# Optimization experiments

Hardware: AMD Instinct MI355X
Metric: run time of the kernel (lower is better)

## Reference

```python
import jax, jax.numpy as jnp
import numpy as np

N_NODES = 50000
N_EDGES = 1600000
D_IN = 512
D_OUT = 512


def setup_inputs() -> dict:
    key = jax.random.key(0)
    k1, k2, k3, k4, k5 = jax.random.split(key, 5)
    inputs = jax.random.normal(k1, (N_NODES, D_IN), dtype=jnp.float32)
    # xavier_uniform for weight [D_IN, D_OUT]
    limit = float(np.sqrt(6.0 / (D_IN + D_OUT)))
    weight = jax.random.uniform(k2, (D_IN, D_OUT), dtype=jnp.float32, minval=-limit, maxval=limit)
    adj_rows = jnp.sort(jax.random.randint(k3, (N_EDGES,), 0, N_NODES, dtype=jnp.int32))
    adj_cols = jax.random.randint(k4, (N_EDGES,), 0, N_NODES, dtype=jnp.int32)
    adj_vals = jax.random.uniform(k5, (N_EDGES,), dtype=jnp.float32)
    return {"inputs": inputs, "weight": weight, "adj_rows": adj_rows,
            "adj_cols": adj_cols, "adj_vals": adj_vals}


def reference(inputs, weight, adj_rows, adj_cols, adj_vals):
    # dropout(p=0.0) is identity in this configuration
    support = inputs @ weight                      # [N, D_OUT] dense GEMM
    gathered = support[adj_cols] * adj_vals[:, None]   # [E, D_OUT]
    output = jax.ops.segment_sum(gathered, adj_rows, num_segments=N_NODES)  # spmm
    return output
```

## Files before the change

### kernel.cpp

```cpp
#include <hip/hip_runtime.h>
#include <hip/hip_bf16.h>

#define N_NODES 50000
#define N_EDGES 1600000
#define D 512

typedef __attribute__((ext_vector_type(8))) short short8;
typedef __attribute__((ext_vector_type(4))) float f32x4;
typedef __attribute__((ext_vector_type(2))) float f32x2;
typedef __attribute__((ext_vector_type(8))) unsigned short u16x8;

__device__ __forceinline__ void async_copy16(const void* g, void* l) {
    __builtin_amdgcn_global_load_lds(
        (const __attribute__((address_space(1))) unsigned int*)g,
        (__attribute__((address_space(3))) unsigned int*)l, 16, 0, 0);
}

__global__ __launch_bounds__(256) void cvt_kernel(const float* __restrict__ X,
                                                  unsigned short* __restrict__ Xb) {
    size_t idx = (size_t)(blockIdx.x * 256 + threadIdx.x) * 8;
    f32x4 v0 = *(const f32x4*)(X + idx);
    f32x4 v1 = *(const f32x4*)(X + idx + 4);
    u16x8 u;
#pragma unroll
    for (int k = 0; k < 4; ++k) {
        u[k]     = __bfloat16_as_ushort(__float2bfloat16(v0[k]));
        u[k + 4] = __bfloat16_as_ushort(__float2bfloat16(v1[k]));
    }
    *(u16x8*)(Xb + idx) = u;
}

__global__ __launch_bounds__(256) void wt_kernel(const float* __restrict__ W,
                                                 unsigned short* __restrict__ Wt) {
    int idx = blockIdx.x * 256 + threadIdx.x;
    int k = idx >> 9;
    int n = idx & 511;
    Wt[n * D + k] = __bfloat16_as_ushort(__float2bfloat16(W[k * D + n]));
}

__global__ __launch_bounds__(256) void rowptr_kernel(const int* __restrict__ rows,
                                                     int* __restrict__ row_start) {
    int r = blockIdx.x * 256 + threadIdx.x;
    if (r > N_NODES) return;
    int lo = 0, hi = N_EDGES;
    while (lo < hi) {
        int mid = (lo + hi) >> 1;
        if (rows[mid] < r) lo = mid + 1; else hi = mid;
    }
    row_start[r] = lo;
}

__global__ __launch_bounds__(256) void gemm_kernel(const unsigned short* __restrict__ Xb,
                                                   const unsigned short* __restrict__ Wt,
                                                   __hip_bfloat16* __restrict__ support) {
    __shared__ unsigned short As[128 * 32];
    __shared__ unsigned short Bs[128 * 32];

    const int t = threadIdx.x;
    const int lane = t & 63;
    const int wave = t >> 6;
    const int wm = (wave & 1) * 64;
    const int wn = (wave >> 1) * 64;
    const int m0 = blockIdx.x * 128;
    const int n0 = blockIdx.y * 128;
    const int l15 = lane & 15;
    const int quad = lane >> 4;

    f32x4 acc[4][4];
#pragma unroll
    for (int i = 0; i < 4; ++i)
#pragma unroll
        for (int j = 0; j < 4; ++j) acc[i][j] = (f32x4)(0.0f);

    const int srow = t >> 2;
    const int skb = (t & 3) * 8;
    int gra = m0 + srow;        if (gra > N_NODES - 1) gra = N_NODES - 1;
    int grb = m0 + 64 + srow;   if (grb > N_NODES - 1) grb = N_NODES - 1;
    const size_t aoff0 = (size_t)gra * D + skb;
    const size_t aoff1 = (size_t)grb * D + skb;
    const size_t boff0 = (size_t)(n0 + srow) * D + skb;
    const size_t boff1 = (size_t)(n0 + 64 + srow) * D + skb;
    unsigned short* lA = As + t * 8;
    unsigned short* lB = Bs + t * 8;

    for (int kt = 0; kt < D / 32; ++kt) {
        const int k0 = kt * 32;
        async_copy16(Xb + aoff0 + k0, lA);
        async_copy16(Xb + aoff1 + k0, lA + 2048);
        async_copy16(Wt + boff0 + k0, lB);
        async_copy16(Wt + boff1 + k0, lB + 2048);
        __syncthreads();

        short8 af[4], bf[4];
#pragma unroll
        for (int i = 0; i < 4; ++i) af[i] = *(const short8*)(As + (wm + i * 16 + l15) * 32 + quad * 8);
#pragma unroll
        for (int j = 0; j < 4; ++j) bf[j] = *(const short8*)(Bs + (wn + j * 16 + l15) * 32 + quad * 8);
#pragma unroll
        for (int i = 0; i < 4; ++i)
#pragma unroll
            for (int j = 0; j < 4; ++j)
                acc[i][j] = __builtin_amdgcn_mfma_f32_16x16x32_bf16(af[i], bf[j], acc[i][j], 0, 0, 0);
        __syncthreads();
    }

#pragma unroll
    for (int i = 0; i < 4; ++i) {
        int grow = m0 + wm + i * 16 + quad * 4;
#pragma unroll
        for (int j = 0; j < 4; ++j) {
            int gc = n0 + wn + j * 16 + l15;
#pragma unroll
            for (int rr = 0; rr < 4; ++rr) {
                int gr = grow + rr;
                if (gr < N_NODES)
                    support[(size_t)gr * D + gc] = __float2bfloat16(acc[i][j][rr]);
            }
        }
    }
}

__global__ __launch_bounds__(256) void spmm_kernel(const unsigned short* __restrict__ support,
                                                   const int* __restrict__ cols,
                                                   const float* __restrict__ vals,
                                                   const int* __restrict__ row_start,
                                                   float* __restrict__ out) {
    const int r = blockIdx.x;
    const int t = threadIdx.x;
    const int s = row_start[r];
    const int e = row_start[r + 1];
    const size_t co = 2 * t;

    float ax = 0.f, ay = 0.f;
    int i = s;
    for (; i + 8 <= e; i += 8) {
        int c[8]; float v[8]; unsigned int h[8];
#pragma unroll
        for (int k = 0; k < 8; ++k) { c[k] = cols[i + k]; v[k] = vals[i + k]; }
#pragma unroll
        for (int k = 0; k < 8; ++k)
            h[k] = *(const unsigned int*)(support + (size_t)c[k] * D + co);
#pragma unroll
        for (int k = 0; k < 8; ++k) {
            ax += v[k] * __uint_as_float(h[k] << 16);
            ay += v[k] * __uint_as_float(h[k] & 0xffff0000u);
        }
    }
    for (; i < e; ++i) {
        int c = cols[i];
        float v = vals[i];
        unsigned int h = *(const unsigned int*)(support + (size_t)c * D + co);
        ax += v * __uint_as_float(h << 16);
        ay += v * __uint_as_float(h & 0xffff0000u);
    }
    f32x2 o; o[0] = ax; o[1] = ay;
    __builtin_nontemporal_store(o, (f32x2*)(out + (size_t)r * D + co));
}

extern "C" void kernel_launch(void* const* d_in, const int* in_sizes, int n_in,
                              void* d_out, int out_size, void* d_ws, size_t ws_size,
                              hipStream_t stream) {
    (void)in_sizes; (void)n_in; (void)out_size; (void)ws_size;
    const float* X    = (const float*)d_in[0];
    const float* W    = (const float*)d_in[1];
    const int* rows   = (const int*)d_in[2];
    const int* cols   = (const int*)d_in[3];
    const float* vals = (const float*)d_in[4];
    float* out = (float*)d_out;

    unsigned short* support = (unsigned short*)d_ws;
    unsigned short* Wt      = support + (size_t)N_NODES * D;
    int* row_start          = (int*)(Wt + (size_t)D * D);
    unsigned short* Xb = (unsigned short*)d_out;

    cvt_kernel<<<12500, 256, 0, stream>>>(X, Xb);
    wt_kernel<<<(D * D) / 256, 256, 0, stream>>>(W, Wt);
    rowptr_kernel<<<(N_NODES + 256) / 256, 256, 0, stream>>>(rows, row_start);

    dim3 gg((N_NODES + 127) / 128, D / 128);
    gemm_kernel<<<gg, 256, 0, stream>>>(Xb, Wt, (__hip_bfloat16*)support);

    spmm_kernel<<<N_NODES, 256, 0, stream>>>(support, cols, vals, row_start, out);
}
```

Baseline: 460.5 us.

## Map one wavefront per row in SpMM with 16-byte gathers

The SpMM kernel now assigns each 64-lane wavefront one output row, with each lane handling 8 columns via 16-byte loads, instead of one 256-thread block per row with 4-byte loads. This cuts the number of edge index/value loads per row by a factor of four and widens the gather transactions. Edges are unrolled by 4 instead of 8, so fewer gathers are in flight per thread. Work may also be less balanced across waves in the same block.

Measured after the change: 473.1 us. 2.7% more time.

```diff
diff --git a/kernel.cpp b/kernel.cpp
--- a/kernel.cpp
+++ b/kernel.cpp
@@ -120,41 +120,54 @@
     }
 }
 
+__device__ __forceinline__ void fma8(float* acc, uint4 h, float v) {
+#pragma unroll
+    for (int d = 0; d < 4; ++d) {
+        unsigned int w = (&h.x)[d];
+        acc[2 * d]     += v * __uint_as_float(w << 16);
+        acc[2 * d + 1] += v * __uint_as_float(w & 0xffff0000u);
+    }
+}
+
 __global__ __launch_bounds__(256) void spmm_kernel(const unsigned short* __restrict__ support,
                                                    const int* __restrict__ cols,
                                                    const float* __restrict__ vals,
                                                    const int* __restrict__ row_start,
                                                    float* __restrict__ out) {
-    const int r = blockIdx.x;
     const int t = threadIdx.x;
+    const int lane = t & 63;
+    const int wave = t >> 6;
+    const int r = blockIdx.x * 4 + wave;
     const int s = row_start[r];
     const int e = row_start[r + 1];
-    const size_t co = 2 * t;
+    const int co = lane * 8;
 
-    float ax = 0.f, ay = 0.f;
+    float acc[8];
+#pragma unroll
+    for (int k = 0; k < 8; ++k) acc[k] = 0.f;
+
     int i = s;
-    for (; i + 8 <= e; i += 8) {
-        int c[8]; float v[8]; unsigned int h[8];
+    for (; i + 4 <= e; i += 4) {
+        int c[4]; float v[4]; uint4 h[4];
 #pragma unroll
-        for (int k = 0; k < 8; ++k) { c[k] = cols[i + k]; v[k] = vals[i + k]; }
+        for (int k = 0; k < 4; ++k) { c[k] = cols[i + k]; v[k] = vals[i + k]; }
 #pragma unroll
-        for (int k = 0; k < 8; ++k)
-            h[k] = *(const unsigned int*)(support + (size_t)c[k] * D + co);
+        for (int k = 0; k < 4; ++k)
+            h[k] = *(const uint4*)(support + (size_t)c[k] * D + co);
 #pragma unroll
-        for (int k = 0; k < 8; ++k) {
-            ax += v[k] * __uint_as_float(h[k] << 16);
-            ay += v[k] * __uint_as_float(h[k] & 0xffff0000u);
-        }
+        for (int k = 0; k < 4; ++k) fma8(acc, h[k], v[k]);
     }
     for (; i < e; ++i) {
-        int c = cols[i];
-        float v = vals[i];
-        unsigned int h = *(const unsigned int*)(support + (size_t)c * D + co);
-        ax += v * __uint_as_float(h << 16);
-        ay += v * __uint_as_float(h & 0xffff0000u);
+        uint4 h = *(const uint4*)(support + (size_t)cols[i] * D + co);
+        fma8(acc, h, vals[i]);
     }
-    f32x2 o; o[0] = ax; o[1] = ay;
-    __builtin_nontemporal_store(o, (f32x2*)(out + (size_t)r * D + co));
+
+    f32x4 o0, o1;
+#pragma unroll
+    for (int k = 0; k < 4; ++k) { o0[k] = acc[k]; o1[k] = acc[k + 4]; }
+    float* op = out + (size_t)r * D + co;
+    __builtin_nontemporal_store(o0, (f32x4*)op);
+    __builtin_nontemporal_store(o1, (f32x4*)(op + 4));
 }
 
 extern "C" void kernel_launch(void* const* d_in, const int* in_sizes, int n_in,
@@ -180,5 +193,5 @@
     dim3 gg((N_NODES + 127) / 128, D / 128);
     gemm_kernel<<<gg, 256, 0, stream>>>(Xb, Wt, (__hip_bfloat16*)support);
 
-    spmm_kernel<<<N_NODES, 256, 0, stream>>>(support, cols, vals, row_start, out);
+    spmm_kernel<<<12500, 256, 0, stream>>>(support, cols, vals, row_start, out);
 }
```

## Fuse fp32-to-bf16 conversion into double-buffered GEMM with 128x256 tiles

Applied to the files above, without the earlier changes.

Drops the separate input conversion kernel. The GEMM now loads fp32 X directly, converts it to bf16 in registers and writes it to LDS. The GEMM also double-buffers its LDS tiles so that next-tile loads overlap the MFMA work, and moves to 512-thread blocks computing 128x256 tiles, which halves the reloads of the X tile. The aim is to remove the round trip of the bf16 X copy through memory and to hide load latency, at the cost of more LDS and register pressure per block.

Result: faster. 446.1 us (-3.1%).

```diff
diff --git a/kernel.cpp b/kernel.cpp
--- a/kernel.cpp
+++ b/kernel.cpp
@@ -14,20 +14,6 @@
     __builtin_amdgcn_global_load_lds(
         (const __attribute__((address_space(1))) unsigned int*)g,
         (__attribute__((address_space(3))) unsigned int*)l, 16, 0, 0);
-}
-
-__global__ __launch_bounds__(256) void cvt_kernel(const float* __restrict__ X,
-                                                  unsigned short* __restrict__ Xb) {
-    size_t idx = (size_t)(blockIdx.x * 256 + threadIdx.x) * 8;
-    f32x4 v0 = *(const f32x4*)(X + idx);
-    f32x4 v1 = *(const f32x4*)(X + idx + 4);
-    u16x8 u;
-#pragma unroll
-    for (int k = 0; k < 4; ++k) {
-        u[k]     = __bfloat16_as_ushort(__float2bfloat16(v0[k]));
-        u[k + 4] = __bfloat16_as_ushort(__float2bfloat16(v1[k]));
-    }
-    *(u16x8*)(Xb + idx) = u;
 }
 
 __global__ __launch_bounds__(256) void wt_kernel(const float* __restrict__ W,
@@ -50,19 +36,24 @@
     row_start[r] = lo;
 }
 
-__global__ __launch_bounds__(256) void gemm_kernel(const unsigned short* __restrict__ Xb,
-                                                   const unsigned short* __restrict__ Wt,
-                                                   __hip_bfloat16* __restrict__ support) {
-    __shared__ unsigned short As[128 * 32];
-    __shared__ unsigned short Bs[128 * 32];
+#define BM 128
+#define BN 256
+#define BK 32
+
+__global__ __launch_bounds__(512, 4) void gemm_kernel(const float* __restrict__ X,
+                                                      const unsigned short* __restrict__ Wt,
+                                                      __hip_bfloat16* __restrict__ support) {
+    __shared__ unsigned short As[2][BM * BK];
+    __shared__ unsigned short Bs[2][BN * BK];
 
     const int t = threadIdx.x;
     const int lane = t & 63;
-    const int wave = t >> 6;
-    const int wm = (wave & 1) * 64;
-    const int wn = (wave >> 1) * 64;
-    const int m0 = blockIdx.x * 128;
-    const int n0 = blockIdx.y * 128;
+    const int w = t >> 6;
+    const int wm = (w >> 2) * 64;
+    const int wn = (w & 3) * 64;
+    const int bid = blockIdx.x;
+    const int m0 = (bid >> 1) * BM;
+    const int n0 = (bid & 1) * BN;
     const int l15 = lane & 15;
     const int quad = lane >> 4;
 
@@ -72,36 +63,69 @@
 #pragma unroll
         for (int j = 0; j < 4; ++j) acc[i][j] = (f32x4)(0.0f);
 
-    const int srow = t >> 2;
-    const int skb = (t & 3) * 8;
-    int gra = m0 + srow;        if (gra > N_NODES - 1) gra = N_NODES - 1;
-    int grb = m0 + 64 + srow;   if (grb > N_NODES - 1) grb = N_NODES - 1;
-    const size_t aoff0 = (size_t)gra * D + skb;
-    const size_t aoff1 = (size_t)grb * D + skb;
-    const size_t boff0 = (size_t)(n0 + srow) * D + skb;
-    const size_t boff1 = (size_t)(n0 + 64 + srow) * D + skb;
-    unsigned short* lA = As + t * 8;
-    unsigned short* lB = Bs + t * 8;
-
-    for (int kt = 0; kt < D / 32; ++kt) {
-        const int k0 = kt * 32;
-        async_copy16(Xb + aoff0 + k0, lA);
-        async_copy16(Xb + aoff1 + k0, lA + 2048);
-        async_copy16(Wt + boff0 + k0, lB);
-        async_copy16(Wt + boff1 + k0, lB + 2048);
-        __syncthreads();
+    int arow = m0 + (t >> 2);
+    if (arow > N_NODES - 1) arow = N_NODES - 1;
+    const float* abase = X + (size_t)arow * D + (t & 3) * 8;
+    const int awr = (t >> 2) * BK + (t & 3) * 8;
+
+
+    {
+        f32x4 a0 = *(const f32x4*)abase;
+        f32x4 a1 = *(const f32x4*)(abase + 4);
+#pragma unroll
+        for (int c = 0; c < 2; ++c) {
+            int cid = c * 512 + t;
+            async_copy16(Wt + (size_t)(n0 + (cid >> 2)) * D + (cid & 3) * 8,
+                         &Bs[0][cid * 8]);
+        }
+        u16x8 u;
+#pragma unroll
+        for (int k = 0; k < 4; ++k) {
+            u[k]     = __bfloat16_as_ushort(__float2bfloat16(a0[k]));
+            u[k + 4] = __bfloat16_as_ushort(__float2bfloat16(a1[k]));
+        }
+        *(u16x8*)(&As[0][awr]) = u;
+    }
+    __syncthreads();
+
+    int cur = 0;
+    for (int kt = 0; kt < D / BK; ++kt) {
+        f32x4 a0n, a1n;
+        const int nxt = cur ^ 1;
+        if (kt < D / BK - 1) {
+            const int k0n = (kt + 1) * BK;
+            a0n = *(const f32x4*)(abase + k0n);
+            a1n = *(const f32x4*)(abase + k0n + 4);
+#pragma unroll
+            for (int c = 0; c < 2; ++c) {
+                int cid = c * 512 + t;
+                async_copy16(Wt + (size_t)(n0 + (cid >> 2)) * D + k0n + (cid & 3) * 8,
+                             &Bs[nxt][cid * 8]);
+            }
+        }
 
         short8 af[4], bf[4];
 #pragma unroll
-        for (int i = 0; i < 4; ++i) af[i] = *(const short8*)(As + (wm + i * 16 + l15) * 32 + quad * 8);
-#pragma unroll
-        for (int j = 0; j < 4; ++j) bf[j] = *(const short8*)(Bs + (wn + j * 16 + l15) * 32 + quad * 8);
+        for (int i = 0; i < 4; ++i) af[i] = *(const short8*)(&As[cur][(wm + i * 16 + l15) * BK + quad * 8]);
+#pragma unroll
+        for (int j = 0; j < 4; ++j) bf[j] = *(const short8*)(&Bs[cur][(wn + j * 16 + l15) * BK + quad * 8]);
 #pragma unroll
         for (int i = 0; i < 4; ++i)
 #pragma unroll
             for (int j = 0; j < 4; ++j)
                 acc[i][j] = __builtin_amdgcn_mfma_f32_16x16x32_bf16(af[i], bf[j], acc[i][j], 0, 0, 0);
+
+        if (kt < D / BK - 1) {
+            u16x8 u;
+#pragma unroll
+            for (int k = 0; k < 4; ++k) {
+                u[k]     = __bfloat16_as_ushort(__float2bfloat16(a0n[k]));
+                u[k + 4] = __bfloat16_as_ushort(__float2bfloat16(a1n[k]));
+            }
+            *(u16x8*)(&As[nxt][awr]) = u;
+        }
         __syncthreads();
+        cur ^= 1;
     }
 
 #pragma unroll
@@ -171,14 +195,12 @@
     unsigned short* support = (unsigned short*)d_ws;
     unsigned short* Wt      = support + (size_t)N_NODES * D;
     int* row_start          = (int*)(Wt + (size_t)D * D);
-    unsigned short* Xb = (unsigned short*)d_out;
-
-    cvt_kernel<<<12500, 256, 0, stream>>>(X, Xb);
+
     wt_kernel<<<(D * D) / 256, 256, 0, stream>>>(W, Wt);
     rowptr_kernel<<<(N_NODES + 256) / 256, 256, 0, stream>>>(rows, row_start);
 
-    dim3 gg((N_NODES + 127) / 128, D / 128);
-    gemm_kernel<<<gg, 256, 0, stream>>>(Xb, Wt, (__hip_bfloat16*)support);
+    const int mblocks = (N_NODES + BM - 1) / BM;
+    gemm_kernel<<<mblocks * 2, 512, 0, stream>>>(X, Wt, (__hip_bfloat16*)support);
 
     spmm_kernel<<<N_NODES, 256, 0, stream>>>(support, cols, vals, row_start, out);
 }
```

## Fuse fp32-to-bf16 conversion into GEMM with full-K LDS A panel and direct B loads

Applied to the files above, without the earlier changes.

Removes the separate X conversion kernel: each GEMM block now loads a 64-row fp32 panel of X, converts it to bf16, and stores the whole K=512 panel in XOR-swizzled LDS. The K-loop then runs without barriers, reading B (Wt) fragments straight from global memory instead of staging them through LDS. Tiles change to 64x256 with 512 threads. This saves a full bf16 write and reread of X, but each of the two N-blocks per panel reads and converts X again, and the B fragments come from uncoalesced global loads that rely on the cache.

After: 508.0 us. 1.1x slower.

```diff
diff --git a/kernel.cpp b/kernel.cpp
--- a/kernel.cpp
+++ b/kernel.cpp
@@ -9,26 +9,6 @@
 typedef __attribute__((ext_vector_type(4))) float f32x4;
 typedef __attribute__((ext_vector_type(2))) float f32x2;
 typedef __attribute__((ext_vector_type(8))) unsigned short u16x8;
-
-__device__ __forceinline__ void async_copy16(const void* g, void* l) {
-    __builtin_amdgcn_global_load_lds(
-        (const __attribute__((address_space(1))) unsigned int*)g,
-        (__attribute__((address_space(3))) unsigned int*)l, 16, 0, 0);
-}
-
-__global__ __launch_bounds__(256) void cvt_kernel(const float* __restrict__ X,
-                                                  unsigned short* __restrict__ Xb) {
-    size_t idx = (size_t)(blockIdx.x * 256 + threadIdx.x) * 8;
-    f32x4 v0 = *(const f32x4*)(X + idx);
-    f32x4 v1 = *(const f32x4*)(X + idx + 4);
-    u16x8 u;
-#pragma unroll
-    for (int k = 0; k < 4; ++k) {
-        u[k]     = __bfloat16_as_ushort(__float2bfloat16(v0[k]));
-        u[k + 4] = __bfloat16_as_ushort(__float2bfloat16(v1[k]));
-    }
-    *(u16x8*)(Xb + idx) = u;
-}
 
 __global__ __launch_bounds__(256) void wt_kernel(const float* __restrict__ W,
                                                  unsigned short* __restrict__ Wt) {
@@ -50,62 +30,73 @@
     row_start[r] = lo;
 }
 
-__global__ __launch_bounds__(256) void gemm_kernel(const unsigned short* __restrict__ Xb,
-                                                   const unsigned short* __restrict__ Wt,
-                                                   __hip_bfloat16* __restrict__ support) {
-    __shared__ unsigned short As[128 * 32];
-    __shared__ unsigned short Bs[128 * 32];
+#define BM 64
+#define BN 256
+
+__global__ __launch_bounds__(512, 2) void gemm_kernel(const float* __restrict__ X,
+                                                      const unsigned short* __restrict__ Wt,
+                                                      __hip_bfloat16* __restrict__ support) {
+    __shared__ unsigned short As[BM * D];
 
     const int t = threadIdx.x;
     const int lane = t & 63;
-    const int wave = t >> 6;
-    const int wm = (wave & 1) * 64;
-    const int wn = (wave >> 1) * 64;
-    const int m0 = blockIdx.x * 128;
-    const int n0 = blockIdx.y * 128;
+    const int w = t >> 6;
+    const int wm = (w >> 2) * 32;
+    const int wn = (w & 3) * 64;
+    const int bid = blockIdx.x;
+    const int m0 = (bid >> 1) * BM;
+    const int n0 = (bid & 1) * BN;
     const int l15 = lane & 15;
     const int quad = lane >> 4;
 
-    f32x4 acc[4][4];
+    f32x4 acc[2][4];
 #pragma unroll
-    for (int i = 0; i < 4; ++i)
+    for (int i = 0; i < 2; ++i)
 #pragma unroll
         for (int j = 0; j < 4; ++j) acc[i][j] = (f32x4)(0.0f);
 
-    const int srow = t >> 2;
-    const int skb = (t & 3) * 8;
-    int gra = m0 + srow;        if (gra > N_NODES - 1) gra = N_NODES - 1;
-    int grb = m0 + 64 + srow;   if (grb > N_NODES - 1) grb = N_NODES - 1;
-    const size_t aoff0 = (size_t)gra * D + skb;
-    const size_t aoff1 = (size_t)grb * D + skb;
-    const size_t boff0 = (size_t)(n0 + srow) * D + skb;
-    const size_t boff1 = (size_t)(n0 + 64 + srow) * D + skb;
-    unsigned short* lA = As + t * 8;
-    unsigned short* lB = Bs + t * 8;
+#pragma unroll
+    for (int it = 0; it < 8; ++it) {
+        const int row = it * 8 + w;
+        int grow = m0 + row;
+        if (grow > N_NODES - 1) grow = N_NODES - 1;
+        const float* src = X + (size_t)grow * D + lane * 8;
+        f32x4 a0 = *(const f32x4*)src;
+        f32x4 a1 = *(const f32x4*)(src + 4);
+        u16x8 u;
+#pragma unroll
+        for (int k = 0; k < 4; ++k) {
+            u[k]     = __bfloat16_as_ushort(__float2bfloat16(a0[k]));
+            u[k + 4] = __bfloat16_as_ushort(__float2bfloat16(a1[k]));
+        }
+        int off = row * D + lane * 8;
+        off ^= (row & 7) << 3;
+        *(u16x8*)(&As[off]) = u;
+    }
+    __syncthreads();
 
+#pragma unroll 4
     for (int kt = 0; kt < D / 32; ++kt) {
-        const int k0 = kt * 32;
-        async_copy16(Xb + aoff0 + k0, lA);
-        async_copy16(Xb + aoff1 + k0, lA + 2048);
-        async_copy16(Wt + boff0 + k0, lB);
-        async_copy16(Wt + boff1 + k0, lB + 2048);
-        __syncthreads();
-
-        short8 af[4], bf[4];
+        short8 af[2], bf[4];
 #pragma unroll
-        for (int i = 0; i < 4; ++i) af[i] = *(const short8*)(As + (wm + i * 16 + l15) * 32 + quad * 8);
+        for (int i = 0; i < 2; ++i) {
+            const int row = wm + i * 16 + l15;
+            int off = row * D + kt * 32 + quad * 8;
+            off ^= (row & 7) << 3;
+            af[i] = *(const short8*)(&As[off]);
+        }
 #pragma unroll
-        for (int j = 0; j < 4; ++j) bf[j] = *(const short8*)(Bs + (wn + j * 16 + l15) * 32 + quad * 8);
+        for (int j = 0; j < 4; ++j)
+            bf[j] = *(const short8*)(Wt + (size_t)(n0 + wn + j * 16 + l15) * D + kt * 32 + quad * 8);
 #pragma unroll
-        for (int i = 0; i < 4; ++i)
+        for (int i = 0; i < 2; ++i)
 #pragma unroll
             for (int j = 0; j < 4; ++j)
                 acc[i][j] = __builtin_amdgcn_mfma_f32_16x16x32_bf16(af[i], bf[j], acc[i][j], 0, 0, 0);
-        __syncthreads();
     }
 
 #pragma unroll
-    for (int i = 0; i < 4; ++i) {
+    for (int i = 0; i < 2; ++i) {
         int grow = m0 + wm + i * 16 + quad * 4;
 #pragma unroll
         for (int j = 0; j < 4; ++j) {
@@ -171,14 +162,12 @@
     unsigned short* support = (unsigned short*)d_ws;
     unsigned short* Wt      = support + (size_t)N_NODES * D;
     int* row_start          = (int*)(Wt + (size_t)D * D);
-    unsigned short* Xb = (unsigned short*)d_out;
 
-    cvt_kernel<<<12500, 256, 0, stream>>>(X, Xb);
     wt_kernel<<<(D * D) / 256, 256, 0, stream>>>(W, Wt);
     rowptr_kernel<<<(N_NODES + 256) / 256, 256, 0, stream>>>(rows, row_start);
 
-    dim3 gg((N_NODES + 127) / 128, D / 128);
-    gemm_kernel<<<gg, 256, 0, stream>>>(Xb, Wt, (__hip_bfloat16*)support);
+    const int mpanels = (N_NODES + BM - 1) / BM;
+    gemm_kernel<<<mpanels * 2, 512, 0, stream>>>(X, Wt, (__hip_bfloat16*)support);
 
     spmm_kernel<<<N_NODES, 256, 0, stream>>>(support, cols, vals, row_start, out);
 }
```
